# Kernel optimization log

Hardware: AMD Instinct MI355X
Metric: run time of the kernel (lower is better)

The kernel has to match this reference:

```python
import jax, jax.numpy as jnp
import numpy as np

T_TAYLOR = 10  # T=10 in OrthogonalGCNConvLayer
N_ORTH_LAYERS = 10


def _taylor_expm(S):
    # exp(S) truncated at T terms; S is skew-symmetric -> approx orthogonal
    I = jnp.eye(S.shape[0], dtype=S.dtype)
    term = I
    acc = I
    for k in range(1, T_TAYLOR + 1):
        term = term @ S / k
        acc = acc + term
    return acc


def setup_inputs() -> dict:
    key = jax.random.key(0)
    ks = jax.random.split(key, 8)
    N = 200_000
    E = 1_200_000
    x = jax.random.normal(ks[0], (N, 1), dtype=jnp.float32)
    edge_index = jax.random.randint(ks[1], (2, E), 0, N, dtype=jnp.int64)
    edge_weight = jax.random.uniform(ks[2], (E,), dtype=jnp.float32)
    W0 = jax.random.normal(ks[3], (1, 64), dtype=jnp.float32) * 0.1
    b0 = jnp.zeros((64,), dtype=jnp.float32)
    # small scale so the truncated matrix exponential stays well-conditioned
    W_orth = jax.random.normal(ks[4], (N_ORTH_LAYERS, 64, 64), dtype=jnp.float32) * 0.05
    W11 = jax.random.normal(ks[5], (64, 1), dtype=jnp.float32) * 0.1
    b11 = jnp.zeros((1,), dtype=jnp.float32)
    return {"x": x, "edge_index": edge_index, "edge_weight": edge_weight,
            "W0": W0, "b0": b0, "W_orth": W_orth, "W11": W11, "b11": b11}


def reference(x, edge_index, edge_weight, W0, b0, W_orth, W11, b11):
    N = x.shape[0]
    row, col = edge_index[0], edge_index[1]
    # add_self_loops=True: append (i,i) edges with weight 1 (PyG gcn_norm fill_value=1)
    loop = jnp.arange(N, dtype=row.dtype)
    row_f = jnp.concatenate([row, loop])
    col_f = jnp.concatenate([col, loop])
    w_f = jnp.concatenate([edge_weight, jnp.ones((N,), dtype=edge_weight.dtype)])
    # degree via scatter-sum over target nodes (matches scatter(..., col, reduce='sum'))
    deg = jax.ops.segment_sum(w_f, col_f, num_segments=N)
    deg_inv_sqrt = jnp.where(deg > 0, jax.lax.rsqrt(jnp.maximum(deg, 1e-30)), 0.0)
    norm = deg_inv_sqrt[row_f] * w_f * deg_inv_sqrt[col_f]  # [E+N]

    def propagate(h):
        # gather messages from source nodes, scale, scatter-add at targets
        return jax.ops.segment_sum(norm[:, None] * h[row_f], col_f, num_segments=N)

    # block 0: GCNConv(1 -> 64)
    h = propagate(x @ W0) + b0
    # blocks 1..10: Orthogonal GCN conv (64 -> 64), Identity activation,
    # no residual / bias; orthogonal weight = truncated expm of skew(W)
    for k in range(N_ORTH_LAYERS):
        Wk = W_orth[k]
        orth = _taylor_expm(Wk - Wk.T)
        h = propagate(h) @ orth
    # block 11: GCNConv(64 -> 1)
    out = propagate(h @ W11) + b11
    return out[:, :, None]  # [N, 1, 1]
```

## Files before the change

kernel.cpp:

```cpp
#include <hip/hip_runtime.h>
#include <hip/hip_bf16.h>


#define TPB 256
#define CSH 11
#define CSZ 2048
#define CAPSH 14
#define FSH 7
#define FBPB 16
#define PE 4096

__device__ void v_part(float* __restrict__ smem,
                       const float* __restrict__ W_orth,
                       const float* __restrict__ W11,
                       const float* __restrict__ W0,
                       const float* __restrict__ b0,
                       float* __restrict__ st,
                       int khi, int klo, bool first) {
    const int l = threadIdx.x;
    if (l >= 64) return;
    float* S  = smem;
    float* tl = smem + 4160;
    float u = first ? W11[l] : st[2 + l];
    for (int k = khi; k >= klo; --k) {
        const float* Wk = W_orth + (size_t)k * 4096;
        #pragma unroll 1
        for (int i = 0; i < 64; ++i)
            S[i * 65 + l] = Wk[i * 64 + l] - Wk[l * 64 + i];
        float term = u, acc = u;
        for (int t = 1; t <= 10; ++t) {
            tl[l] = term;
            float p = 0.f;
            #pragma unroll 16
            for (int j = 0; j < 64; ++j)
                p = fmaf(S[l * 65 + j], tl[j], p);
            term = p / (float)t;
            acc += term;
        }
        u = acc;
    }
    if (klo == 0) {
        float a = W0[l] * u, b = b0[l] * u;
        #pragma unroll
        for (int off = 32; off; off >>= 1) {
            a += __shfl_down(a, off);
            b += __shfl_down(b, off);
        }
        if (l == 0) { st[0] = a; st[1] = b; }
    } else {
        st[2 + l] = u;
    }
}

__global__ __launch_bounds__(1024) void k_part(
        const int* __restrict__ ei, const float* __restrict__ w,
        int E, int nchunk, int CB,
        int* __restrict__ pos, int2* __restrict__ recA,
        const float* __restrict__ W_orth,
        const float* __restrict__ W11, float* __restrict__ scal) {
    __shared__ float smem[9216];
    __shared__ int hist[128], rank[128], gbase[128];
    __shared__ int sscan[128], starts[129];
    const int me = blockIdx.x, t = threadIdx.x;
    if (me == nchunk) { v_part(smem, W_orth, W11, nullptr, nullptr, scal, 9, 4, true); return; }
    int2* staged = (int2*)smem;
    unsigned char* sb = (unsigned char*)(smem + 8192);
    if (t < 128) { hist[t] = 0; rank[t] = 0; }
    __syncthreads();
    const int e0 = me * PE, e1 = min(E, e0 + PE);
    const int nE = e1 - e0;
    const int nv = nE >> 2;
    const int4*   cv4 = (const int4*)(ei + (size_t)E + e0);
    const int4*   sv4 = (const int4*)(ei + e0);
    const float4* wv4 = (const float4*)(w + e0);
    for (int g = t; g < nv; g += 1024) {
        int4 c4 = cv4[g];
        atomicAdd(&hist[c4.x >> CSH], 1);
        atomicAdd(&hist[c4.y >> CSH], 1);
        atomicAdd(&hist[c4.z >> CSH], 1);
        atomicAdd(&hist[c4.w >> CSH], 1);
    }
    for (int e = e0 + (nv << 2) + t; e < e1; e += 1024)
        atomicAdd(&hist[ei[E + e] >> CSH], 1);
    __syncthreads();
    if (t < 128) sscan[t] = hist[t];
    __syncthreads();
    for (int o = 1; o < 128; o <<= 1) {
        int v = (t < 128 && t >= o) ? sscan[t - o] : 0;
        __syncthreads();
        if (t < 128) sscan[t] += v;
        __syncthreads();
    }
    if (t < 128) starts[t] = sscan[t] - hist[t];
    if (t == 127) starts[128] = sscan[127];
    if (t < CB && hist[t] > 0)
        gbase[t] = (t << CAPSH) + atomicAdd(&pos[t], hist[t]);
    __syncthreads();
    for (int g = t; g < nv; g += 1024) {
        int4 s4 = sv4[g]; int4 c4 = cv4[g]; float4 w4 = wv4[g];
        int b, r, p;
        b = c4.x >> CSH; r = atomicAdd(&rank[b], 1); p = starts[b] + r;
        staged[p] = make_int2(s4.x | ((c4.x & (CSZ - 1)) << 18), __float_as_int(w4.x)); sb[p] = (unsigned char)b;
        b = c4.y >> CSH; r = atomicAdd(&rank[b], 1); p = starts[b] + r;
        staged[p] = make_int2(s4.y | ((c4.y & (CSZ - 1)) << 18), __float_as_int(w4.y)); sb[p] = (unsigned char)b;
        b = c4.z >> CSH; r = atomicAdd(&rank[b], 1); p = starts[b] + r;
        staged[p] = make_int2(s4.z | ((c4.z & (CSZ - 1)) << 18), __float_as_int(w4.z)); sb[p] = (unsigned char)b;
        b = c4.w >> CSH; r = atomicAdd(&rank[b], 1); p = starts[b] + r;
        staged[p] = make_int2(s4.w | ((c4.w & (CSZ - 1)) << 18), __float_as_int(w4.w)); sb[p] = (unsigned char)b;
    }
    for (int e = e0 + (nv << 2) + t; e < e1; e += 1024) {
        int src = ei[e], c = ei[E + e];
        int b = c >> CSH;
        int r = atomicAdd(&rank[b], 1);
        int p = starts[b] + r;
        staged[p] = make_int2(src | ((c & (CSZ - 1)) << 18), __float_as_int(w[e]));
        sb[p] = (unsigned char)b;
    }
    __syncthreads();
    for (int s = t; s < nE; s += 1024) {
        int b = sb[s];
        recA[gbase[b] + (s - starts[b])] = staged[s];
    }
}

__global__ __launch_bounds__(1024) void k_sub(
        const int* __restrict__ pos, const int2* __restrict__ recA,
        int2* __restrict__ recB,
        int* __restrict__ binStart, int* __restrict__ binEnd,
        const float* __restrict__ x, float* __restrict__ dis,
        float* __restrict__ d2, float* __restrict__ u0,
        int N, int CB,
        const float* __restrict__ W_orth,
        const float* __restrict__ W0, const float* __restrict__ b0,
        float* __restrict__ scal) {
    __shared__ float smem[6656];
    __shared__ int hw[16][17];
    __shared__ int h16[16], st16[17], run16[16], rk16[16], bst16[17], bcnt[16];
    const int b = blockIdx.x, t = threadIdx.x;
    if (b == CB) { v_part(smem, W_orth, nullptr, W0, b0, scal, 3, 0, false); return; }
    int2* staged = (int2*)smem;
    float* acc   = smem + 4096;
    unsigned char* sb = (unsigned char*)(smem + 6144);
    const int wid = t >> 6;
    const int cnt = pos[b];
    const int2* rin = recA + ((size_t)b << CAPSH);
    int2* rout      = recB + ((size_t)b << CAPSH);
    for (int i = t; i < CSZ; i += 1024) acc[i] = 0.f;
    if (t < 272) ((int*)hw)[t] = 0;
    __syncthreads();
    for (int k = t; k < cnt; k += 1024) {
        int2 rc = rin[k];
        int cl = rc.x >> 18;
        atomicAdd(&hw[wid][cl >> FSH], 1);
        atomicAdd(&acc[cl], __int_as_float(rc.y));
    }
    __syncthreads();
    if (t < 16) { int s = 0; for (int q = 0; q < 16; ++q) s += hw[q][t]; h16[t] = s; }
    __syncthreads();
    if (t == 0) { int s = 0; for (int j = 0; j < 16; ++j) { st16[j] = s; s += h16[j]; } st16[16] = s; }
    __syncthreads();
    if (t < 16) {
        binStart[b * FBPB + t] = (b << CAPSH) + st16[t];
        binEnd  [b * FBPB + t] = (b << CAPSH) + st16[t + 1];
        run16[t] = st16[t];
    }
    for (int i = t; i < CSZ; i += 1024) {
        int node = (b << CSH) + i;
        if (node < N) {
            float deg = 1.0f + acc[i];
            float ds = rsqrtf(deg);
            dis[node] = ds;
            d2[node]  = 1.0f / deg;
            u0[node]  = ds * x[node];
        }
    }
    __syncthreads();
    for (int base = 0; base < cnt; base += 2048) {
        const int n = min(2048, cnt - base);
        if (t < 272) ((int*)hw)[t] = 0;
        __syncthreads();
        for (int k = base + t; k < base + n; k += 1024)
            atomicAdd(&hw[wid][(rin[k].x >> 18) >> FSH], 1);
        __syncthreads();
        if (t < 16) { int s = 0; for (int q = 0; q < 16; ++q) s += hw[q][t]; bcnt[t] = s; rk16[t] = 0; }
        __syncthreads();
        if (t == 0) { int s = 0; for (int j = 0; j < 16; ++j) { bst16[j] = s; s += bcnt[j]; } bst16[16] = s; }
        __syncthreads();
        for (int k = base + t; k < base + n; k += 1024) {
            int2 rc = rin[k];
            int cl = rc.x >> 18;
            int j = cl >> FSH;
            int r = atomicAdd(&rk16[j], 1);
            int p = bst16[j] + r;
            staged[p] = make_int2((rc.x & 0x3FFFF) | ((cl & 127) << 18), rc.y);
            sb[p] = (unsigned char)j;
        }
        __syncthreads();
        for (int s = t; s < n; s += 1024) {
            int j = sb[s];
            rout[run16[j] + (s - bst16[j])] = staged[s];
        }
        __syncthreads();
        if (t < 16) run16[t] += bcnt[t];
        __syncthreads();
    }
}

__global__ void k_gather(const int* __restrict__ binStart,
                         const int* __restrict__ binEnd,
                         const int2* __restrict__ rec,
                         const float* __restrict__ d2,
                         const float* __restrict__ pv, float* __restrict__ cv,
                         int N, int mode,
                         const float* __restrict__ scal,
                         const float* __restrict__ dis,
                         const float* __restrict__ b11, float* __restrict__ out) {
    const int fb = blockIdx.x, t = threadIdx.x;
    __shared__ float acc[128];
    if (t < 128) acc[t] = 0.f;
    __syncthreads();
    const int k0 = binStart[fb], k1 = binEnd[fb];
    for (int k = k0 + t; k < k1; k += TPB) {
        int2 rc = rec[k];
        atomicAdd(&acc[rc.x >> 18],
                  __int_as_float(rc.y) * pv[rc.x & 0x3FFFF]);
    }
    __syncthreads();
    if (t < 128) {
        int i = (fb << FSH) + t;
        if (i < N) {
            float up = d2[i] * (pv[i] + acc[t]);
            if (mode == 1)
                cv[i] = scal[0] * up + scal[1] * dis[i];
            else if (mode == 2)
                out[i] = up / dis[i] + b11[0];
            else
                cv[i] = up;
        }
    }
}

extern "C" void kernel_launch(void* const* d_in, const int* in_sizes, int n_in,
                              void* d_out, int out_size, void* d_ws, size_t ws_size,
                              hipStream_t stream) {
    const float* x      = (const float*)d_in[0];
    const int*   ei     = (const int*)d_in[1];
    const float* w      = (const float*)d_in[2];
    const float* W0     = (const float*)d_in[3];
    const float* b0     = (const float*)d_in[4];
    const float* W_orth = (const float*)d_in[5];
    const float* W11    = (const float*)d_in[6];
    const float* b11    = (const float*)d_in[7];

    const int N = in_sizes[0];
    const int E = in_sizes[2];
    const int CB = (N + CSZ - 1) >> CSH;
    const int nchunk = (E + PE - 1) / PE;
    const size_t cap = (size_t)CB << CAPSH;

    char* ws = (char*)d_ws;
    int2*  recA     = (int2*)ws;   ws += cap * 8;
    int2*  recB     = (int2*)ws;   ws += cap * 8;
    float* uA       = (float*)ws;  ws += (size_t)N * 4;
    float* uB       = (float*)ws;  ws += (size_t)N * 4;
    float* dis      = (float*)ws;  ws += (size_t)N * 4;
    float* d2       = (float*)ws;  ws += (size_t)N * 4;
    int*   binStart = (int*)ws;    ws += (size_t)CB * FBPB * 4;
    int*   binEnd   = (int*)ws;    ws += (size_t)CB * FBPB * 4;
    int*   pos      = (int*)ws;    ws += 128 * 4;
    float* scal     = (float*)ws;  ws += 80 * 4;

    hipMemsetAsync(pos, 0, 128 * 4, stream);
    k_part<<<nchunk + 1, 1024, 0, stream>>>(ei, w, E, nchunk, CB, pos, recA,
                                            W_orth, W11, scal);
    k_sub<<<CB + 1, 1024, 0, stream>>>(pos, recA, recB, binStart, binEnd,
                                       x, dis, d2, uA, N, CB,
                                       W_orth, W0, b0, scal);

    float* prev = uA;
    float* cur  = uB;
    for (int it = 0; it < 12; ++it) {
        int mode = (it == 0) ? 1 : (it == 11 ? 2 : 0);
        k_gather<<<CB * FBPB, TPB, 0, stream>>>(binStart, binEnd, recB, d2,
                                                prev, cur, N, mode, scal, dis,
                                                b11, (float*)d_out);
        float* tmp = prev; prev = cur; cur = tmp;
    }
}
```

Baseline: 309.3 us.

## Parallelize second-level bucketing across many blocks and hold skew matrix in registers

The single-block-per-coarse-bin sub-sort is split into eight blocks per bin, each handling a 2048-record batch and appending to fixed-capacity fine bins through atomic counters. Degree computation moves into its own kernel that reads the fine bins. The whole 10-layer orthogonal vector chain now runs in one block inside the partition kernel, with the skew row kept in registers and the dot product split into four accumulators. The partition kernel uses 512-thread blocks over 2048-edge chunks. The aim is to remove the serialized per-bin loop in k_sub, at the cost of one extra kernel launch, a fixed per-bin capacity of 1024 that could overflow on skewed graphs, and a longer serial chain in one block.

```diff
diff --git a/kernel.cpp b/kernel.cpp
--- a/kernel.cpp
+++ b/kernel.cpp
@@ -7,64 +7,69 @@
 #define CSZ 2048
 #define CAPSH 14
 #define FSH 7
-#define FBPB 16
-#define PE 4096
-
-__device__ void v_part(float* __restrict__ smem,
-                       const float* __restrict__ W_orth,
-                       const float* __restrict__ W11,
-                       const float* __restrict__ W0,
-                       const float* __restrict__ b0,
-                       float* __restrict__ st,
-                       int khi, int klo, bool first) {
+#define CAPF 1024
+#define PE 2048
+#define PTPB 512
+#define BATCH 2048
+
+__device__ void v_chain_reg(float* __restrict__ smem,
+                            const float* __restrict__ W_orth,
+                            const float* __restrict__ W11,
+                            const float* __restrict__ W0,
+                            const float* __restrict__ b0,
+                            float* __restrict__ st) {
     const int l = threadIdx.x;
     if (l >= 64) return;
-    float* S  = smem;
+    float* Wl = smem;
     float* tl = smem + 4160;
-    float u = first ? W11[l] : st[2 + l];
-    for (int k = khi; k >= klo; --k) {
+    float u = W11[l];
+    float sreg[64];
+    for (int k = 9; k >= 0; --k) {
         const float* Wk = W_orth + (size_t)k * 4096;
-        #pragma unroll 1
+        #pragma unroll 8
         for (int i = 0; i < 64; ++i)
-            S[i * 65 + l] = Wk[i * 64 + l] - Wk[l * 64 + i];
+            Wl[i * 65 + l] = Wk[i * 64 + l];
+        #pragma unroll
+        for (int j = 0; j < 64; ++j)
+            sreg[j] = Wl[l * 65 + j] - Wl[j * 65 + l];
         float term = u, acc = u;
         for (int t = 1; t <= 10; ++t) {
             tl[l] = term;
-            float p = 0.f;
-            #pragma unroll 16
-            for (int j = 0; j < 64; ++j)
-                p = fmaf(S[l * 65 + j], tl[j], p);
-            term = p / (float)t;
+            float p0 = 0.f, p1 = 0.f, p2 = 0.f, p3 = 0.f;
+            #pragma unroll
+            for (int j = 0; j < 16; ++j) {
+                p0 = fmaf(sreg[j],      tl[j],      p0);
+                p1 = fmaf(sreg[j + 16], tl[j + 16], p1);
+                p2 = fmaf(sreg[j + 32], tl[j + 32], p2);
+                p3 = fmaf(sreg[j + 48], tl[j + 48], p3);
+            }
+            term = ((p0 + p1) + (p2 + p3)) / (float)t;
             acc += term;
         }
         u = acc;
     }
-    if (klo == 0) {
-        float a = W0[l] * u, b = b0[l] * u;
-        #pragma unroll
-        for (int off = 32; off; off >>= 1) {
-            a += __shfl_down(a, off);
-            b += __shfl_down(b, off);
-        }
-        if (l == 0) { st[0] = a; st[1] = b; }
-    } else {
-        st[2 + l] = u;
-    }
-}
-
-__global__ __launch_bounds__(1024) void k_part(
+    float a = W0[l] * u, b = b0[l] * u;
+    #pragma unroll
+    for (int off = 32; off; off >>= 1) {
+        a += __shfl_down(a, off);
+        b += __shfl_down(b, off);
+    }
+    if (l == 0) { st[0] = a; st[1] = b; }
+}
+
+__global__ __launch_bounds__(PTPB) void k_part(
         const int* __restrict__ ei, const float* __restrict__ w,
         int E, int nchunk, int CB,
         int* __restrict__ pos, int2* __restrict__ recA,
-        const float* __restrict__ W_orth,
-        const float* __restrict__ W11, float* __restrict__ scal) {
-    __shared__ float smem[9216];
-    __shared__ int hist[128], rank[128], gbase[128];
-    __shared__ int sscan[128], starts[129];
+        const float* __restrict__ W_orth, const float* __restrict__ W11,
+        const float* __restrict__ W0, const float* __restrict__ b0,
+        float* __restrict__ scal) {
+    __shared__ float smem[4608];
+    __shared__ int hist[128], rank[128], gbase[128], sscan[128], starts[129];
     const int me = blockIdx.x, t = threadIdx.x;
-    if (me == nchunk) { v_part(smem, W_orth, W11, nullptr, nullptr, scal, 9, 4, true); return; }
+    if (me == nchunk) { v_chain_reg(smem, W_orth, W11, W0, b0, scal); return; }
     int2* staged = (int2*)smem;
-    unsigned char* sb = (unsigned char*)(smem + 8192);
+    unsigned char* sb = (unsigned char*)(smem + 4096);
     if (t < 128) { hist[t] = 0; rank[t] = 0; }
     __syncthreads();
     const int e0 = me * PE, e1 = min(E, e0 + PE);
@@ -73,14 +78,14 @@
     const int4*   cv4 = (const int4*)(ei + (size_t)E + e0);
     const int4*   sv4 = (const int4*)(ei + e0);
     const float4* wv4 = (const float4*)(w + e0);
-    for (int g = t; g < nv; g += 1024) {
+    for (int g = t; g < nv; g += PTPB) {
         int4 c4 = cv4[g];
         atomicAdd(&hist[c4.x >> CSH], 1);
         atomicAdd(&hist[c4.y >> CSH], 1);
         atomicAdd(&hist[c4.z >> CSH], 1);
         atomicAdd(&hist[c4.w >> CSH], 1);
     }
-    for (int e = e0 + (nv << 2) + t; e < e1; e += 1024)
+    for (int e = e0 + (nv << 2) + t; e < e1; e += PTPB)
         atomicAdd(&hist[ei[E + e] >> CSH], 1);
     __syncthreads();
     if (t < 128) sscan[t] = hist[t];
@@ -96,7 +101,7 @@
     if (t < CB && hist[t] > 0)
         gbase[t] = (t << CAPSH) + atomicAdd(&pos[t], hist[t]);
     __syncthreads();
-    for (int g = t; g < nv; g += 1024) {
+    for (int g = t; g < nv; g += PTPB) {
         int4 s4 = sv4[g]; int4 c4 = cv4[g]; float4 w4 = wv4[g];
         int b, r, p;
         b = c4.x >> CSH; r = atomicAdd(&rank[b], 1); p = starts[b] + r;
@@ -108,7 +113,7 @@
         b = c4.w >> CSH; r = atomicAdd(&rank[b], 1); p = starts[b] + r;
         staged[p] = make_int2(s4.w | ((c4.w & (CSZ - 1)) << 18), __float_as_int(w4.w)); sb[p] = (unsigned char)b;
     }
-    for (int e = e0 + (nv << 2) + t; e < e1; e += 1024) {
+    for (int e = e0 + (nv << 2) + t; e < e1; e += PTPB) {
         int src = ei[e], c = ei[E + e];
         int b = c >> CSH;
         int r = atomicAdd(&rank[b], 1);
@@ -117,98 +122,89 @@
         sb[p] = (unsigned char)b;
     }
     __syncthreads();
-    for (int s = t; s < nE; s += 1024) {
+    for (int s = t; s < nE; s += PTPB) {
         int b = sb[s];
         recA[gbase[b] + (s - starts[b])] = staged[s];
     }
 }
 
-__global__ __launch_bounds__(1024) void k_sub(
+__global__ __launch_bounds__(PTPB) void k_subP(
         const int* __restrict__ pos, const int2* __restrict__ recA,
-        int2* __restrict__ recB,
-        int* __restrict__ binStart, int* __restrict__ binEnd,
-        const float* __restrict__ x, float* __restrict__ dis,
-        float* __restrict__ d2, float* __restrict__ u0,
-        int N, int CB,
-        const float* __restrict__ W_orth,
-        const float* __restrict__ W0, const float* __restrict__ b0,
-        float* __restrict__ scal) {
-    __shared__ float smem[6656];
-    __shared__ int hw[16][17];
-    __shared__ int h16[16], st16[17], run16[16], rk16[16], bst16[17], bcnt[16];
-    const int b = blockIdx.x, t = threadIdx.x;
-    if (b == CB) { v_part(smem, W_orth, nullptr, W0, b0, scal, 3, 0, false); return; }
-    int2* staged = (int2*)smem;
-    float* acc   = smem + 4096;
-    unsigned char* sb = (unsigned char*)(smem + 6144);
+        int* __restrict__ binPos, int2* __restrict__ recB) {
+    __shared__ int2 staged[BATCH];
+    __shared__ unsigned char sb[BATCH];
+    __shared__ int hw[8][20];
+    __shared__ int bcnt[16], bst16[17], rk16[16], gb[16];
+    const int blk = blockIdx.x, t = threadIdx.x;
+    const int b = blk >> 3, j = blk & 7;
+    const int cnt = pos[b];
+    const int base = j * BATCH;
+    const int n = min(BATCH, cnt - base);
+    if (n <= 0) return;
+    const int2* rin = recA + ((size_t)b << CAPSH) + base;
     const int wid = t >> 6;
-    const int cnt = pos[b];
-    const int2* rin = recA + ((size_t)b << CAPSH);
-    int2* rout      = recB + ((size_t)b << CAPSH);
-    for (int i = t; i < CSZ; i += 1024) acc[i] = 0.f;
-    if (t < 272) ((int*)hw)[t] = 0;
-    __syncthreads();
-    for (int k = t; k < cnt; k += 1024) {
+    if (t < 160) ((int*)hw)[t] = 0;
+    __syncthreads();
+    for (int k = t; k < n; k += PTPB)
+        atomicAdd(&hw[wid][(rin[k].x >> 18) >> FSH], 1);
+    __syncthreads();
+    if (t < 16) {
+        int s = 0;
+        #pragma unroll
+        for (int q = 0; q < 8; ++q) s += hw[q][t];
+        bcnt[t] = s; rk16[t] = 0;
+    }
+    __syncthreads();
+    if (t == 0) {
+        int s = 0;
+        for (int q = 0; q < 16; ++q) { bst16[q] = s; s += bcnt[q]; }
+        bst16[16] = s;
+    }
+    __syncthreads();
+    if (t < 16 && bcnt[t] > 0)
+        gb[t] = ((blk >> 3 << 4) + t) * CAPF + atomicAdd(&binPos[(b << 4) + t], bcnt[t]);
+    __syncthreads();
+    for (int k = t; k < n; k += PTPB) {
         int2 rc = rin[k];
         int cl = rc.x >> 18;
-        atomicAdd(&hw[wid][cl >> FSH], 1);
-        atomicAdd(&acc[cl], __int_as_float(rc.y));
-    }
-    __syncthreads();
-    if (t < 16) { int s = 0; for (int q = 0; q < 16; ++q) s += hw[q][t]; h16[t] = s; }
-    __syncthreads();
-    if (t == 0) { int s = 0; for (int j = 0; j < 16; ++j) { st16[j] = s; s += h16[j]; } st16[16] = s; }
-    __syncthreads();
-    if (t < 16) {
-        binStart[b * FBPB + t] = (b << CAPSH) + st16[t];
-        binEnd  [b * FBPB + t] = (b << CAPSH) + st16[t + 1];
-        run16[t] = st16[t];
-    }
-    for (int i = t; i < CSZ; i += 1024) {
-        int node = (b << CSH) + i;
-        if (node < N) {
-            float deg = 1.0f + acc[i];
+        int f = cl >> FSH;
+        int r = atomicAdd(&rk16[f], 1);
+        int p = bst16[f] + r;
+        staged[p] = make_int2((rc.x & 0x3FFFF) | ((cl & 127) << 18), rc.y);
+        sb[p] = (unsigned char)f;
+    }
+    __syncthreads();
+    for (int s = t; s < n; s += PTPB) {
+        int f = sb[s];
+        recB[gb[f] + (s - bst16[f])] = staged[s];
+    }
+}
+
+__global__ void k_deg(const int* __restrict__ binPos, const int2* __restrict__ recB,
+                      const float* __restrict__ x, float* __restrict__ dis,
+                      float* __restrict__ d2, float* __restrict__ u0, int N) {
+    const int fb = blockIdx.x, t = threadIdx.x;
+    __shared__ float acc[128];
+    if (t < 128) acc[t] = 0.f;
+    __syncthreads();
+    const int cnt = binPos[fb];
+    const int2* r = recB + (size_t)fb * CAPF;
+    for (int k = t; k < cnt; k += TPB)
+        atomicAdd(&acc[r[k].x >> 18], __int_as_float(r[k].y));
+    __syncthreads();
+    if (t < 128) {
+        int i = (fb << FSH) + t;
+        if (i < N) {
+            float deg = 1.0f + acc[t];
             float ds = rsqrtf(deg);
-            dis[node] = ds;
-            d2[node]  = 1.0f / deg;
-            u0[node]  = ds * x[node];
+            dis[i] = ds;
+            d2[i]  = 1.0f / deg;
+            u0[i]  = ds * x[i];
         }
     }
-    __syncthreads();
-    for (int base = 0; base < cnt; base += 2048) {
-        const int n = min(2048, cnt - base);
-        if (t < 272) ((int*)hw)[t] = 0;
-        __syncthreads();
-        for (int k = base + t; k < base + n; k += 1024)
-            atomicAdd(&hw[wid][(rin[k].x >> 18) >> FSH], 1);
-        __syncthreads();
-        if (t < 16) { int s = 0; for (int q = 0; q < 16; ++q) s += hw[q][t]; bcnt[t] = s; rk16[t] = 0; }
-        __syncthreads();
-        if (t == 0) { int s = 0; for (int j = 0; j < 16; ++j) { bst16[j] = s; s += bcnt[j]; } bst16[16] = s; }
-        __syncthreads();
-        for (int k = base + t; k < base + n; k += 1024) {
-            int2 rc = rin[k];
-            int cl = rc.x >> 18;
-            int j = cl >> FSH;
-            int r = atomicAdd(&rk16[j], 1);
-            int p = bst16[j] + r;
-            staged[p] = make_int2((rc.x & 0x3FFFF) | ((cl & 127) << 18), rc.y);
-            sb[p] = (unsigned char)j;
-        }
-        __syncthreads();
-        for (int s = t; s < n; s += 1024) {
-            int j = sb[s];
-            rout[run16[j] + (s - bst16[j])] = staged[s];
-        }
-        __syncthreads();
-        if (t < 16) run16[t] += bcnt[t];
-        __syncthreads();
-    }
-}
-
-__global__ void k_gather(const int* __restrict__ binStart,
-                         const int* __restrict__ binEnd,
-                         const int2* __restrict__ rec,
+}
+
+__global__ void k_gather(const int* __restrict__ binPos, const int2* __restrict__ rec,
                          const float* __restrict__ d2,
                          const float* __restrict__ pv, float* __restrict__ cv,
                          int N, int mode,
@@ -219,9 +215,10 @@
     __shared__ float acc[128];
     if (t < 128) acc[t] = 0.f;
     __syncthreads();
-    const int k0 = binStart[fb], k1 = binEnd[fb];
-    for (int k = k0 + t; k < k1; k += TPB) {
-        int2 rc = rec[k];
+    const int cnt = binPos[fb];
+    const int2* r = rec + (size_t)fb * CAPF;
+    for (int k = t; k < cnt; k += TPB) {
+        int2 rc = r[k];
         atomicAdd(&acc[rc.x >> 18],
                   __int_as_float(rc.y) * pv[rc.x & 0x3FFFF]);
     }
@@ -255,35 +252,34 @@
     const int N = in_sizes[0];
     const int E = in_sizes[2];
     const int CB = (N + CSZ - 1) >> CSH;
+    const int NFB = CB << 4;
     const int nchunk = (E + PE - 1) / PE;
-    const size_t cap = (size_t)CB << CAPSH;
+    const size_t capA = (size_t)CB << CAPSH;
+    const size_t capB = (size_t)NFB * CAPF;
 
     char* ws = (char*)d_ws;
-    int2*  recA     = (int2*)ws;   ws += cap * 8;
-    int2*  recB     = (int2*)ws;   ws += cap * 8;
-    float* uA       = (float*)ws;  ws += (size_t)N * 4;
-    float* uB       = (float*)ws;  ws += (size_t)N * 4;
-    float* dis      = (float*)ws;  ws += (size_t)N * 4;
-    float* d2       = (float*)ws;  ws += (size_t)N * 4;
-    int*   binStart = (int*)ws;    ws += (size_t)CB * FBPB * 4;
-    int*   binEnd   = (int*)ws;    ws += (size_t)CB * FBPB * 4;
-    int*   pos      = (int*)ws;    ws += 128 * 4;
-    float* scal     = (float*)ws;  ws += 80 * 4;
-
-    hipMemsetAsync(pos, 0, 128 * 4, stream);
-    k_part<<<nchunk + 1, 1024, 0, stream>>>(ei, w, E, nchunk, CB, pos, recA,
-                                            W_orth, W11, scal);
-    k_sub<<<CB + 1, 1024, 0, stream>>>(pos, recA, recB, binStart, binEnd,
-                                       x, dis, d2, uA, N, CB,
-                                       W_orth, W0, b0, scal);
+    int2*  recA   = (int2*)ws;   ws += capA * 8;
+    int2*  recB   = (int2*)ws;   ws += capB * 8;
+    float* uA     = (float*)ws;  ws += (size_t)N * 4;
+    float* uB     = (float*)ws;  ws += (size_t)N * 4;
+    float* dis    = (float*)ws;  ws += (size_t)N * 4;
+    float* d2     = (float*)ws;  ws += (size_t)N * 4;
+    int*   pos    = (int*)ws;    ws += 128 * 4;
+    int*   binPos = (int*)ws;    ws += (size_t)NFB * 4;
+    float* scal   = (float*)ws;  ws += 80 * 4;
+
+    hipMemsetAsync(pos, 0, (128 + (size_t)NFB) * 4, stream);
+    k_part<<<nchunk + 1, PTPB, 0, stream>>>(ei, w, E, nchunk, CB, pos, recA,
+                                            W_orth, W11, W0, b0, scal);
+    k_subP<<<CB * 8, PTPB, 0, stream>>>(pos, recA, binPos, recB);
+    k_deg<<<NFB, TPB, 0, stream>>>(binPos, recB, x, dis, d2, uA, N);
 
     float* prev = uA;
     float* cur  = uB;
     for (int it = 0; it < 12; ++it) {
         int mode = (it == 0) ? 1 : (it == 11 ? 2 : 0);
-        k_gather<<<CB * FBPB, TPB, 0, stream>>>(binStart, binEnd, recB, d2,
-                                                prev, cur, N, mode, scal, dis,
-                                                b11, (float*)d_out);
+        k_gather<<<NFB, TPB, 0, stream>>>(binPos, recB, d2, prev, cur, N,
+                                          mode, scal, dis, b11, (float*)d_out);
         float* tmp = prev; prev = cur; cur = tmp;
     }
 }
```

After: 362.3 us. 1.17x slower.
